# Kernel optimization log

Measured on AMD Instinct MI355X. Metric: run time of the kernel, lower is better.

Reference implementation:

```python
import jax, jax.numpy as jnp
import numpy as np

B, C, CE, H, W = 4, 128, 64, 64, 64
V = H * W
# parent(i) < i//2 guarantees depth <= ceil(log2(V)) = 12; 14 is a safe static bound
MAX_LEVELS = 14


def _gather_v(x, idx):
    # x: [B, C, V], idx: [B, V] -> gather along vertex dim (broadcast over C)
    return jnp.take_along_axis(x, idx[:, None, :], axis=2)


def _tree_filter(feature_in, embed_in, sorted_index, sorted_parent, node_level):
    Bv, Cv, Hv, Wv = feature_in.shape
    Vv = Hv * Wv
    f = feature_in.reshape(Bv, Cv, Vv)
    e = embed_in.reshape(Bv, embed_in.shape[1], Vv)
    # build_edge_weight: gather to BFS order, gather parent, squared-L2 distance, exp(-d)
    f_s = _gather_v(f, sorted_index)          # [B,C,V] features in topological order
    e_s = _gather_v(e, sorted_index)
    e_p = _gather_v(e_s, sorted_parent)
    d2 = jnp.sum((e_s - e_p) ** 2, axis=1)    # [B,V]
    w = jnp.exp(-d2)                          # edge weight node->parent (root: exp(0)=1, unused)
    wB = w[:, None, :]
    # ---- up sweep (leaves -> root), level-parallel over BFS levels ----
    # A_i = f_i + sum_{c in child(i)} w_c * A_c ; Z_i = 1 + sum w_c * Z_c (self_weight = 1)
    aggr_up = f_s
    nrm_up = jnp.ones((Bv, Vv), feature_in.dtype)
    for d in range(MAX_LEVELS - 1, 0, -1):
        mw = jnp.where(node_level == d, w, jnp.zeros((), feature_in.dtype))
        aggr_up = jax.vmap(lambda a, p, m: a.at[:, p].add(m))(
            aggr_up, sorted_parent, mw[:, None, :] * aggr_up)
        nrm_up = jax.vmap(lambda a, p, m: a.at[p].add(m))(
            nrm_up, sorted_parent, mw * nrm_up)
    # ---- down sweep (root -> leaves) ----
    # Ahat_i = A_i + w_i * (Ahat_parent - w_i * A_i); root keeps A_root
    aggr = aggr_up
    nrm = nrm_up
    for d in range(1, MAX_LEVELS):
        sel = node_level == d
        pa = _gather_v(aggr, sorted_parent)
        aggr = jnp.where(sel[:, None, :], aggr_up + wB * (pa - wB * aggr_up), aggr)
        pn = jnp.take_along_axis(nrm, sorted_parent, axis=1)
        nrm = jnp.where(sel, nrm_up + w * (pn - w * nrm_up), nrm)
    out_s = aggr / nrm[:, None, :]
    # scatter back from BFS order to original vertex order
    out = jax.vmap(lambda o, i: jnp.zeros_like(o).at[:, i].set(o))(out_s, sorted_index)
    return out.reshape(Bv, Cv, Hv, Wv)


def setup_inputs() -> dict:
    key = jax.random.key(0)
    k1, k2 = jax.random.split(key)
    feature_in = jax.random.normal(k1, (B, C, H, W), dtype=jnp.float32)
    embed_in = 0.1 * jax.random.normal(k2, (B, CE, H, W), dtype=jnp.float32)
    rng = np.random.default_rng(0)
    sorted_index = np.stack([rng.permutation(V) for _ in range(B)]).astype(np.int32)
    sorted_parent = np.zeros((B, V), dtype=np.int32)
    node_level = np.zeros((B, V), dtype=np.int32)
    for b in range(B):
        for i in range(1, V):
            p = int(rng.integers(0, max(1, i // 2)))  # parent earlier in order, depth <= log2(V)
            sorted_parent[b, i] = p
            node_level[b, i] = node_level[b, p] + 1
    return {
        "feature_in": feature_in,
        "embed_in": embed_in,
        "sorted_index": jnp.asarray(sorted_index),
        "sorted_parent": jnp.asarray(sorted_parent),
        "node_level": jnp.asarray(node_level),
    }


def reference(feature_in, embed_in, sorted_index, sorted_parent, node_level):
    return _tree_filter(feature_in, embed_in, sorted_index, sorted_parent, node_level)
```

## Files before the change

kernel.cpp:

```cpp
#include <hip/hip_runtime.h>

#define BB 4
#define CC 128
#define CE 64
#define VV 4096
#define NLEV 14


__device__ __forceinline__ void lds_fadd(float* p, float v) {
    unsafeAtomicAdd(p, v);
}

__global__ __launch_bounds__(256) void prep_kernel(
    const float* __restrict__ embed,
    const int* __restrict__ sorted_index,
    const int* __restrict__ sorted_parent,
    const int* __restrict__ node_level,
    float* __restrict__ wsort,
    int*   __restrict__ giInv,
    int2*  __restrict__ cpl,
    int*   __restrict__ offs)
{
    int tid = threadIdx.x;
    if (blockIdx.x < BB) {
        int b = blockIdx.x;
        __shared__ int  pos_s[VV];
        __shared__ int4 cntv[NLEV * 64];
        __shared__ int  tot[NLEV];
        __shared__ int  offSh[NLEV + 1];
        int* cnt = (int*)cntv;
        const int* lev = node_level    + b * VV;
        const int* si  = sorted_index  + b * VV;
        const int* par = sorted_parent + b * VV;
        int lane = tid & 63;
        int w    = tid >> 6;

        int dreg[16], sreg[16];
        #pragma unroll
        for (int t = 0; t < 4; ++t) {
            int4 dv = ((const int4*)lev)[tid * 4 + t];
            int4 sv = ((const int4*)si)[tid * 4 + t];
            #pragma unroll
            for (int j = 0; j < 4; ++j) {
                int d = (&dv.x)[j]; d = d < NLEV - 1 ? d : NLEV - 1;
                dreg[t * 4 + j] = d;
                sreg[t * 4 + j] = (&sv.x)[j];
            }
        }

        int rank[16];
        #pragma unroll
        for (int m = 0; m < 16; ++m) {
            int r = 0;
            #pragma unroll
            for (int m2 = 0; m2 < m; ++m2) r += (dreg[m2] == dreg[m]) ? 1 : 0;
            rank[m] = r;
        }

        #pragma unroll
        for (int d = 0; d < NLEV; ++d) {
            int c = 0;
            #pragma unroll
            for (int m = 0; m < 16; ++m) c += (dreg[m] == d) ? 1 : 0;
            cnt[d * 256 + tid] = c;
        }
        __syncthreads();

        for (int d = w; d < NLEV; d += 4) {
            int base = d * 64 + lane;
            int4 cv = cntv[base];
            int ls = cv.x + cv.y + cv.z + cv.w;
            int x = ls;
            #pragma unroll
            for (int off = 1; off < 64; off <<= 1) {
                int y = __shfl_up(x, off, 64);
                if (lane >= off) x += y;
            }
            int excl = x - ls;
            int4 ov;
            ov.x = excl;
            ov.y = excl + cv.x;
            ov.z = excl + cv.x + cv.y;
            ov.w = excl + cv.x + cv.y + cv.z;
            cntv[base] = ov;
            if (lane == 63) tot[d] = x;
        }
        __syncthreads();
        if (tid == 0) {
            int acc = 0;
            for (int d = 0; d < NLEV; ++d) { offSh[d] = acc; acc += tot[d]; }
            offSh[NLEV] = acc;
        }
        __syncthreads();
        if (tid <= NLEV) offs[b * 16 + tid] = offSh[tid];

        int kreg[16];
        #pragma unroll
        for (int m = 0; m < 16; ++m) {
            int d = dreg[m];
            int k = offSh[d] + cnt[d * 256 + tid] + rank[m];
            kreg[m] = k;
            pos_s[16 * tid + m] = k;
            giInv[b * VV + sreg[m]] = k;
        }
        __syncthreads();

        #pragma unroll
        for (int t = 0; t < 4; ++t) {
            int4 pv = ((const int4*)par)[tid * 4 + t];
            #pragma unroll
            for (int j = 0; j < 4; ++j) {
                int m = t * 4 + j;
                int p = (&pv.x)[j];
                cpl[b * VV + kreg[m]] = make_int2(pos_s[p], 16 * tid + m);
            }
        }
    } else {
        __shared__ float part[4][64];
        int bb   = blockIdx.x - BB;
        int b    = bb >> 6;
        int n0   = (bb & 63) << 6;
        int lane = tid & 63;
        int w    = tid >> 6;
        int i    = n0 + lane;
        int vi = sorted_index[b * VV + i];
        int p  = sorted_parent[b * VV + i];
        int vp = sorted_index[b * VV + p];
        const float* eb = embed + (size_t)b * CE * VV;
        float acc = 0.f;
        #pragma unroll
        for (int r = 0; r < 16; ++r) {
            int ce = w * 16 + r;
            float d = eb[ce * VV + vi] - eb[ce * VV + vp];
            acc = fmaf(d, d, acc);
        }
        part[w][lane] = acc;
        __syncthreads();
        if (w == 0) {
            float d2 = part[0][lane] + part[1][lane] + part[2][lane] + part[3][lane];
            wsort[b * VV + i] = __expf(-d2);
        }
    }
}

__global__ __launch_bounds__(512) void tree2_kernel(
    const float* __restrict__ feat,
    const float* __restrict__ wsort,
    const int*  __restrict__ giInv,
    const int2* __restrict__ cpl,
    const int*  __restrict__ offs,
    float* __restrict__ out)
{
    __shared__ float val0[VV];
    __shared__ float val1[VV];
    __shared__ float nrm[VV];
    __shared__ int   cw[VV];
    __shared__ int   offS[16];
    int b   = blockIdx.x >> 6;
    int c0  = (blockIdx.x & 63) << 1;
    int tid = threadIdx.x;

    const int2*  cplB = cpl   + b * VV;
    const int*   ivB  = giInv + b * VV;
    const float* wsB  = wsort + b * VV;
    const float* f0   = feat + ((size_t)(b * CC + c0)) * VV;
    const float* f1   = f0 + VV;

    if (tid < 16) offS[tid] = offs[b * 16 + tid];

    #pragma unroll
    for (int t = 0; t < 8; ++t) {
        int k = tid + t * 512;
        int2 x = cplB[k];
        int wb = __float_as_int(wsB[x.y]);
        cw[k] = (wb & 0xFFFFF000) | x.x;
    }

    int4 kkR[2];
    #pragma unroll
    for (int t = 0; t < 2; ++t) {
        int idx = tid + t * 512;
        int4   kk = ((const int4*)ivB)[idx];
        float4 a  = ((const float4*)f0)[idx];
        float4 bq = ((const float4*)f1)[idx];
        kkR[t] = kk;
        val0[kk.x] = a.x;  val0[kk.y] = a.y;  val0[kk.z] = a.z;  val0[kk.w] = a.w;
        val1[kk.x] = bq.x; val1[kk.y] = bq.y; val1[kk.z] = bq.z; val1[kk.w] = bq.w;
        nrm[kk.x] = 1.f;   nrm[kk.y] = 1.f;   nrm[kk.z] = 1.f;   nrm[kk.w] = 1.f;
    }
    __syncthreads();

    for (int d = NLEV - 1; d >= 1; --d) {
        int s = offS[d], e = offS[d + 1];
        if (s == e) continue;
        for (int k = s + tid; k < e; k += 512) {
            int x = cw[k];
            float w = __int_as_float(x & 0xFFFFF000);
            int  cp = x & 0xFFF;
            lds_fadd(&val0[cp], w * val0[k]);
            lds_fadd(&val1[cp], w * val1[k]);
            lds_fadd(&nrm[cp],  w * nrm[k]);
        }
        __syncthreads();
    }

    for (int d = 1; d <= NLEV - 1; ++d) {
        int s = offS[d], e = offS[d + 1];
        if (s == e) continue;
        for (int k = s + tid; k < e; k += 512) {
            int x = cw[k];
            float w = __int_as_float(x & 0xFFFFF000);
            int  cp = x & 0xFFF;
            float u0 = val0[k], u1 = val1[k], un = nrm[k];
            val0[k] = fmaf(w, fmaf(-w, u0, val0[cp]), u0);
            val1[k] = fmaf(w, fmaf(-w, u1, val1[cp]), u1);
            nrm[k]  = fmaf(w, fmaf(-w, un, nrm[cp]),  un);
        }
        __syncthreads();
    }

    float* o0 = out + ((size_t)(b * CC + c0)) * VV;
    float* o1 = o0 + VV;
    #pragma unroll
    for (int t = 0; t < 2; ++t) {
        int idx = tid + t * 512;
        int4 kk = kkR[t];
        float i0 = __fdividef(1.f, nrm[kk.x]);
        float i1 = __fdividef(1.f, nrm[kk.y]);
        float i2 = __fdividef(1.f, nrm[kk.z]);
        float i3 = __fdividef(1.f, nrm[kk.w]);
        float4 r0, r1;
        r0.x = val0[kk.x] * i0; r0.y = val0[kk.y] * i1;
        r0.z = val0[kk.z] * i2; r0.w = val0[kk.w] * i3;
        r1.x = val1[kk.x] * i0; r1.y = val1[kk.y] * i1;
        r1.z = val1[kk.z] * i2; r1.w = val1[kk.w] * i3;
        ((float4*)o0)[idx] = r0;
        ((float4*)o1)[idx] = r1;
    }
}

extern "C" void kernel_launch(void* const* d_in, const int* in_sizes, int n_in,
                              void* d_out, int out_size, void* d_ws, size_t ws_size,
                              hipStream_t stream) {
    const float* feat          = (const float*)d_in[0];
    const float* embed         = (const float*)d_in[1];
    const int*   sorted_index  = (const int*)d_in[2];
    const int*   sorted_parent = (const int*)d_in[3];
    const int*   node_level    = (const int*)d_in[4];
    float* out = (float*)d_out;

    char* ws = (char*)d_ws;
    const size_t A = (size_t)BB * VV * 4;
    float* wsort = (float*)(ws);
    int*   giInv = (int*)  (ws + A);
    int2*  cpl   = (int2*) (ws + 2 * A);
    int*   offs  = (int*)  (ws + 4 * A);

    prep_kernel<<<BB + BB * 64, 256, 0, stream>>>(
        embed, sorted_index, sorted_parent, node_level, wsort, giInv, cpl, offs);

    tree2_kernel<<<BB * CC / 2, 512, 0, stream>>>(
        feat, wsort, giInv, cpl, offs, out);
}
```

Baseline: 103.3 us.

## Share tree normalizer across channel blocks and fuse edge-weight compute into tree kernel

```diff
diff --git a/kernel.cpp b/kernel.cpp
--- a/kernel.cpp
+++ b/kernel.cpp
@@ -10,20 +10,31 @@
 __device__ __forceinline__ void lds_fadd(float* p, float v) {
     unsafeAtomicAdd(p, v);
 }
+__device__ __forceinline__ float agent_loadf(const float* p) {
+    return __hip_atomic_load(p, __ATOMIC_RELAXED, __HIP_MEMORY_SCOPE_AGENT);
+}
+__device__ __forceinline__ void agent_storef(float* p, float v) {
+    __hip_atomic_store(p, v, __ATOMIC_RELAXED, __HIP_MEMORY_SCOPE_AGENT);
+}
+__device__ __forceinline__ int agent_loadi(const int* p) {
+    return __hip_atomic_load(p, __ATOMIC_RELAXED, __HIP_MEMORY_SCOPE_AGENT);
+}
 
 __global__ __launch_bounds__(256) void prep_kernel(
     const float* __restrict__ embed,
     const int* __restrict__ sorted_index,
     const int* __restrict__ sorted_parent,
     const int* __restrict__ node_level,
-    float* __restrict__ wsort,
     int*   __restrict__ giInv,
     int2*  __restrict__ cpl,
-    int*   __restrict__ offs)
+    int*   __restrict__ offs,
+    int*   __restrict__ sync,
+    float* __restrict__ embedT)
 {
     int tid = threadIdx.x;
     if (blockIdx.x < BB) {
         int b = blockIdx.x;
+        if (tid == 0) { sync[b] = 0; sync[4 + b] = 0; }
         __shared__ int  pos_s[VV];
         __shared__ int4 cntv[NLEV * 64];
         __shared__ int  tot[NLEV];
@@ -47,7 +58,6 @@
                 sreg[t * 4 + j] = (&sv.x)[j];
             }
         }
-
         int rank[16];
         #pragma unroll
         for (int m = 0; m < 16; ++m) {
@@ -56,7 +66,6 @@
             for (int m2 = 0; m2 < m; ++m2) r += (dreg[m2] == dreg[m]) ? 1 : 0;
             rank[m] = r;
         }
-
         #pragma unroll
         for (int d = 0; d < NLEV; ++d) {
             int c = 0;
@@ -65,7 +74,6 @@
             cnt[d * 256 + tid] = c;
         }
         __syncthreads();
-
         for (int d = w; d < NLEV; d += 4) {
             int base = d * 64 + lane;
             int4 cv = cntv[base];
@@ -93,7 +101,6 @@
         }
         __syncthreads();
         if (tid <= NLEV) offs[b * 16 + tid] = offSh[tid];
-
         int kreg[16];
         #pragma unroll
         for (int m = 0; m < 16; ++m) {
@@ -104,7 +111,6 @@
             giInv[b * VV + sreg[m]] = k;
         }
         __syncthreads();
-
         #pragma unroll
         for (int t = 0; t < 4; ++t) {
             int4 pv = ((const int4*)par)[tid * 4 + t];
@@ -116,77 +122,195 @@
             }
         }
     } else {
-        __shared__ float part[4][64];
-        int bb   = blockIdx.x - BB;
-        int b    = bb >> 6;
-        int n0   = (bb & 63) << 6;
-        int lane = tid & 63;
-        int w    = tid >> 6;
-        int i    = n0 + lane;
-        int vi = sorted_index[b * VV + i];
-        int p  = sorted_parent[b * VV + i];
-        int vp = sorted_index[b * VV + p];
-        const float* eb = embed + (size_t)b * CE * VV;
-        float acc = 0.f;
-        #pragma unroll
-        for (int r = 0; r < 16; ++r) {
-            int ce = w * 16 + r;
-            float d = eb[ce * VV + vi] - eb[ce * VV + vp];
-            acc = fmaf(d, d, acc);
-        }
-        part[w][lane] = acc;
-        __syncthreads();
-        if (w == 0) {
-            float d2 = part[0][lane] + part[1][lane] + part[2][lane] + part[3][lane];
-            wsort[b * VV + i] = __expf(-d2);
-        }
-    }
-}
-
-__global__ __launch_bounds__(512) void tree2_kernel(
+        __shared__ float tile[64][65];
+        int tb = blockIdx.x - BB;
+        int b  = tb >> 6;
+        int v0 = (tb & 63) << 6;
+        const float* eb  = embed  + (size_t)b * CE * VV;
+        float*       ebT = embedT + (size_t)b * VV * CE;
+        int cv = tid & 63;
+        int rh = tid >> 6;
+        #pragma unroll
+        for (int it = 0; it < 16; ++it) {
+            int ce = it * 4 + rh;
+            tile[cv][ce] = eb[(size_t)ce * VV + v0 + cv];
+        }
+        __syncthreads();
+        #pragma unroll
+        for (int it = 0; it < 16; ++it) {
+            int dv = it * 4 + rh;
+            ebT[(size_t)(v0 + dv) * CE + cv] = tile[dv][cv];
+        }
+    }
+}
+
+__global__ __launch_bounds__(512, 4) void tree2_kernel(
     const float* __restrict__ feat,
-    const float* __restrict__ wsort,
+    const float* __restrict__ embedT,
+    const int*  __restrict__ sorted_index,
+    const int*  __restrict__ sorted_parent,
+    float* __restrict__ wsort,
     const int*  __restrict__ giInv,
     const int2* __restrict__ cpl,
     const int*  __restrict__ offs,
+    int*   __restrict__ sync,
+    float* __restrict__ nrmInv,
     float* __restrict__ out)
 {
     __shared__ float val0[VV];
     __shared__ float val1[VV];
-    __shared__ float nrm[VV];
     __shared__ int   cw[VV];
     __shared__ int   offS[16];
-    int b   = blockIdx.x >> 6;
-    int c0  = (blockIdx.x & 63) << 1;
     int tid = threadIdx.x;
+
+    if (blockIdx.x < BB) {
+        int b = blockIdx.x;
+        const int2* cplB = cpl + b * VV;
+        if (tid < 16) offS[tid] = offs[b * 16 + tid];
+        #pragma unroll
+        for (int t = 0; t < 8; ++t) {
+            int k = tid + t * 512;
+            int2 x = cplB[k];
+            cw[k] = x.x | (x.y << 12);
+        }
+        if (tid == 0) {
+            while (agent_loadi(&sync[b]) < 64) __builtin_amdgcn_s_sleep(1);
+        }
+        __syncthreads();
+        __threadfence();
+        #pragma unroll
+        for (int t = 0; t < 8; ++t) {
+            int k = tid + t * 512;
+            val0[k] = agent_loadf(&wsort[b * VV + k]);
+        }
+        __syncthreads();
+        #pragma unroll
+        for (int t = 0; t < 8; ++t) {
+            int k = tid + t * 512;
+            int pk = cw[k];
+            int iy = (pk >> 12) & 0xFFF;
+            int wb = __float_as_int(val0[iy]);
+            cw[k] = (wb & 0xFFFFF000) | (pk & 0xFFF);
+        }
+        __syncthreads();
+        #pragma unroll
+        for (int t = 0; t < 8; ++t) val0[tid + t * 512] = 1.f;
+        __syncthreads();
+        for (int d = NLEV - 1; d >= 1; --d) {
+            int s = offS[d], e = offS[d + 1];
+            if (s == e) continue;
+            for (int k = s + tid; k < e; k += 512) {
+                int x = cw[k];
+                float w = __int_as_float(x & 0xFFFFF000);
+                int  cp = x & 0xFFF;
+                lds_fadd(&val0[cp], w * val0[k]);
+            }
+            __syncthreads();
+        }
+        for (int d = 1; d <= NLEV - 1; ++d) {
+            int s = offS[d], e = offS[d + 1];
+            if (s == e) continue;
+            for (int k = s + tid; k < e; k += 512) {
+                int x = cw[k];
+                float w = __int_as_float(x & 0xFFFFF000);
+                int  cp = x & 0xFFF;
+                float un = val0[k];
+                val0[k] = fmaf(w, fmaf(-w, un, val0[cp]), un);
+            }
+            __syncthreads();
+        }
+        #pragma unroll
+        for (int t = 0; t < 8; ++t) {
+            int k = tid + t * 512;
+            agent_storef(&nrmInv[b * VV + k], __fdividef(1.f, val0[k]));
+        }
+        __threadfence();
+        __syncthreads();
+        if (tid == 0) __hip_atomic_store(&sync[4 + b], 1, __ATOMIC_RELAXED, __HIP_MEMORY_SCOPE_AGENT);
+        return;
+    }
+
+    int tb = blockIdx.x - BB;
+    int b  = tb >> 6;
+    int j  = tb & 63;
+    int c0 = j << 1;
 
     const int2*  cplB = cpl   + b * VV;
     const int*   ivB  = giInv + b * VV;
-    const float* wsB  = wsort + b * VV;
     const float* f0   = feat + ((size_t)(b * CC + c0)) * VV;
     const float* f1   = f0 + VV;
 
+    {
+        int n   = tid >> 3;
+        int sub = tid & 7;
+        int i   = (j << 6) + n;
+        int vi = sorted_index[b * VV + i];
+        int p  = sorted_parent[b * VV + i];
+        int vp = sorted_index[b * VV + p];
+        const float4* ra = (const float4*)(embedT + ((size_t)b * VV + vi) * CE);
+        const float4* rb = (const float4*)(embedT + ((size_t)b * VV + vp) * CE);
+        float4 a0 = ra[sub * 2], a1 = ra[sub * 2 + 1];
+        float4 b0 = rb[sub * 2], b1 = rb[sub * 2 + 1];
+        float d2 = 0.f, t0;
+        t0 = a0.x - b0.x; d2 = fmaf(t0, t0, d2);
+        t0 = a0.y - b0.y; d2 = fmaf(t0, t0, d2);
+        t0 = a0.z - b0.z; d2 = fmaf(t0, t0, d2);
+        t0 = a0.w - b0.w; d2 = fmaf(t0, t0, d2);
+        t0 = a1.x - b1.x; d2 = fmaf(t0, t0, d2);
+        t0 = a1.y - b1.y; d2 = fmaf(t0, t0, d2);
+        t0 = a1.z - b1.z; d2 = fmaf(t0, t0, d2);
+        t0 = a1.w - b1.w; d2 = fmaf(t0, t0, d2);
+        d2 += __shfl_xor(d2, 1, 64);
+        d2 += __shfl_xor(d2, 2, 64);
+        d2 += __shfl_xor(d2, 4, 64);
+        if (sub == 0) agent_storef(&wsort[b * VV + i], __expf(-d2));
+    }
+    __threadfence();
+    __syncthreads();
+    if (tid == 0) __hip_atomic_fetch_add(&sync[b], 1, __ATOMIC_RELAXED, __HIP_MEMORY_SCOPE_AGENT);
+
     if (tid < 16) offS[tid] = offs[b * 16 + tid];
-
+    int4   kkR[2];
+    float4 fA[2], fB[2];
+    #pragma unroll
+    for (int t = 0; t < 2; ++t) {
+        int idx = tid + t * 512;
+        kkR[t] = ((const int4*)ivB)[idx];
+        fA[t]  = ((const float4*)f0)[idx];
+        fB[t]  = ((const float4*)f1)[idx];
+    }
     #pragma unroll
     for (int t = 0; t < 8; ++t) {
         int k = tid + t * 512;
         int2 x = cplB[k];
-        int wb = __float_as_int(wsB[x.y]);
-        cw[k] = (wb & 0xFFFFF000) | x.x;
-    }
-
-    int4 kkR[2];
+        cw[k] = x.x | (x.y << 12);
+    }
+
+    if (tid == 0) {
+        while (agent_loadi(&sync[b]) < 64) __builtin_amdgcn_s_sleep(1);
+    }
+    __syncthreads();
+    __threadfence();
+    #pragma unroll
+    for (int t = 0; t < 8; ++t) {
+        int k = tid + t * 512;
+        val0[k] = agent_loadf(&wsort[b * VV + k]);
+    }
+    __syncthreads();
+    #pragma unroll
+    for (int t = 0; t < 8; ++t) {
+        int k = tid + t * 512;
+        int pk = cw[k];
+        int iy = (pk >> 12) & 0xFFF;
+        int wb = __float_as_int(val0[iy]);
+        cw[k] = (wb & 0xFFFFF000) | (pk & 0xFFF);
+    }
+    __syncthreads();
     #pragma unroll
     for (int t = 0; t < 2; ++t) {
-        int idx = tid + t * 512;
-        int4   kk = ((const int4*)ivB)[idx];
-        float4 a  = ((const float4*)f0)[idx];
-        float4 bq = ((const float4*)f1)[idx];
-        kkR[t] = kk;
-        val0[kk.x] = a.x;  val0[kk.y] = a.y;  val0[kk.z] = a.z;  val0[kk.w] = a.w;
-        val1[kk.x] = bq.x; val1[kk.y] = bq.y; val1[kk.z] = bq.z; val1[kk.w] = bq.w;
-        nrm[kk.x] = 1.f;   nrm[kk.y] = 1.f;   nrm[kk.z] = 1.f;   nrm[kk.w] = 1.f;
+        int4 kk = kkR[t];
+        val0[kk.x] = fA[t].x; val0[kk.y] = fA[t].y; val0[kk.z] = fA[t].z; val0[kk.w] = fA[t].w;
+        val1[kk.x] = fB[t].x; val1[kk.y] = fB[t].y; val1[kk.z] = fB[t].z; val1[kk.w] = fB[t].w;
     }
     __syncthreads();
 
@@ -199,11 +323,9 @@
             int  cp = x & 0xFFF;
             lds_fadd(&val0[cp], w * val0[k]);
             lds_fadd(&val1[cp], w * val1[k]);
-            lds_fadd(&nrm[cp],  w * nrm[k]);
-        }
-        __syncthreads();
-    }
-
+        }
+        __syncthreads();
+    }
     for (int d = 1; d <= NLEV - 1; ++d) {
         int s = offS[d], e = offS[d + 1];
         if (s == e) continue;
@@ -211,13 +333,25 @@
             int x = cw[k];
             float w = __int_as_float(x & 0xFFFFF000);
             int  cp = x & 0xFFF;
-            float u0 = val0[k], u1 = val1[k], un = nrm[k];
+            float u0 = val0[k], u1 = val1[k];
             val0[k] = fmaf(w, fmaf(-w, u0, val0[cp]), u0);
             val1[k] = fmaf(w, fmaf(-w, u1, val1[cp]), u1);
-            nrm[k]  = fmaf(w, fmaf(-w, un, nrm[cp]),  un);
-        }
-        __syncthreads();
-    }
+        }
+        __syncthreads();
+    }
+
+    if (tid == 0) {
+        while (agent_loadi(&sync[4 + b]) == 0) __builtin_amdgcn_s_sleep(1);
+    }
+    __syncthreads();
+    __threadfence();
+    float* nv = (float*)cw;
+    #pragma unroll
+    for (int t = 0; t < 8; ++t) {
+        int k = tid + t * 512;
+        nv[k] = agent_loadf(&nrmInv[b * VV + k]);
+    }
+    __syncthreads();
 
     float* o0 = out + ((size_t)(b * CC + c0)) * VV;
     float* o1 = o0 + VV;
@@ -225,10 +359,7 @@
     for (int t = 0; t < 2; ++t) {
         int idx = tid + t * 512;
         int4 kk = kkR[t];
-        float i0 = __fdividef(1.f, nrm[kk.x]);
-        float i1 = __fdividef(1.f, nrm[kk.y]);
-        float i2 = __fdividef(1.f, nrm[kk.z]);
-        float i3 = __fdividef(1.f, nrm[kk.w]);
+        float i0 = nv[kk.x], i1 = nv[kk.y], i2 = nv[kk.z], i3 = nv[kk.w];
         float4 r0, r1;
         r0.x = val0[kk.x] * i0; r0.y = val0[kk.y] * i1;
         r0.z = val0[kk.z] * i2; r0.w = val0[kk.w] * i3;
@@ -251,14 +382,17 @@
 
     char* ws = (char*)d_ws;
     const size_t A = (size_t)BB * VV * 4;
-    float* wsort = (float*)(ws);
-    int*   giInv = (int*)  (ws + A);
-    int2*  cpl   = (int2*) (ws + 2 * A);
-    int*   offs  = (int*)  (ws + 4 * A);
-
-    prep_kernel<<<BB + BB * 64, 256, 0, stream>>>(
-        embed, sorted_index, sorted_parent, node_level, wsort, giInv, cpl, offs);
-
-    tree2_kernel<<<BB * CC / 2, 512, 0, stream>>>(
-        feat, wsort, giInv, cpl, offs, out);
-}
+    float* wsort  = (float*)(ws);
+    int*   giInv  = (int*)  (ws + A);
+    int2*  cpl    = (int2*) (ws + 2 * A);
+    int*   offs   = (int*)  (ws + 4 * A);
+    int*   sync   = (int*)  (ws + 4 * A + 4096);
+    float* nrmInv = (float*)(ws + 5 * A);
+    float* embedT = (float*)(ws + 6 * A);
+
+    prep_kernel<<<BB + 256, 256, 0, stream>>>(
+        embed, sorted_index, sorted_parent, node_level, giInv, cpl, offs, sync, embedT);
+
+    tree2_kernel<<<BB + 256, 512, 0, stream>>>(
+        feat, embedT, sorted_index, sorted_parent, wsort, giInv, cpl, offs, sync, nrmInv, out);
+}
```

After: 205.3 us. 98.7% more time.

## Process one channel per block and prefetch next tree level's edges

Applied to the files above, without the earlier changes.

```diff
diff --git a/kernel.cpp b/kernel.cpp
--- a/kernel.cpp
+++ b/kernel.cpp
@@ -47,7 +47,6 @@
                 sreg[t * 4 + j] = (&sv.x)[j];
             }
         }
-
         int rank[16];
         #pragma unroll
         for (int m = 0; m < 16; ++m) {
@@ -56,7 +55,6 @@
             for (int m2 = 0; m2 < m; ++m2) r += (dreg[m2] == dreg[m]) ? 1 : 0;
             rank[m] = r;
         }
-
         #pragma unroll
         for (int d = 0; d < NLEV; ++d) {
             int c = 0;
@@ -65,7 +63,6 @@
             cnt[d * 256 + tid] = c;
         }
         __syncthreads();
-
         for (int d = w; d < NLEV; d += 4) {
             int base = d * 64 + lane;
             int4 cv = cntv[base];
@@ -93,7 +90,6 @@
         }
         __syncthreads();
         if (tid <= NLEV) offs[b * 16 + tid] = offSh[tid];
-
         int kreg[16];
         #pragma unroll
         for (int m = 0; m < 16; ++m) {
@@ -104,7 +100,6 @@
             giInv[b * VV + sreg[m]] = k;
         }
         __syncthreads();
-
         #pragma unroll
         for (int t = 0; t < 4; ++t) {
             int4 pv = ((const int4*)par)[tid * 4 + t];
@@ -143,7 +138,7 @@
     }
 }
 
-__global__ __launch_bounds__(512) void tree2_kernel(
+__global__ __launch_bounds__(512, 4) void tree1_kernel(
     const float* __restrict__ feat,
     const float* __restrict__ wsort,
     const int*  __restrict__ giInv,
@@ -151,20 +146,18 @@
     const int*  __restrict__ offs,
     float* __restrict__ out)
 {
-    __shared__ float val0[VV];
-    __shared__ float val1[VV];
+    __shared__ float val[VV];
     __shared__ float nrm[VV];
     __shared__ int   cw[VV];
     __shared__ int   offS[16];
-    int b   = blockIdx.x >> 6;
-    int c0  = (blockIdx.x & 63) << 1;
+    int b   = blockIdx.x >> 7;
+    int c   = blockIdx.x & 127;
     int tid = threadIdx.x;
 
     const int2*  cplB = cpl   + b * VV;
     const int*   ivB  = giInv + b * VV;
     const float* wsB  = wsort + b * VV;
-    const float* f0   = feat + ((size_t)(b * CC + c0)) * VV;
-    const float* f1   = f0 + VV;
+    const float* f0   = feat + ((size_t)(b * CC + c)) * VV;
 
     if (tid < 16) offS[tid] = offs[b * 16 + tid];
 
@@ -174,6 +167,7 @@
         int2 x = cplB[k];
         int wb = __float_as_int(wsB[x.y]);
         cw[k] = (wb & 0xFFFFF000) | x.x;
+        nrm[k] = 1.f;
     }
 
     int4 kkR[2];
@@ -182,60 +176,84 @@
         int idx = tid + t * 512;
         int4   kk = ((const int4*)ivB)[idx];
         float4 a  = ((const float4*)f0)[idx];
-        float4 bq = ((const float4*)f1)[idx];
         kkR[t] = kk;
-        val0[kk.x] = a.x;  val0[kk.y] = a.y;  val0[kk.z] = a.z;  val0[kk.w] = a.w;
-        val1[kk.x] = bq.x; val1[kk.y] = bq.y; val1[kk.z] = bq.z; val1[kk.w] = bq.w;
-        nrm[kk.x] = 1.f;   nrm[kk.y] = 1.f;   nrm[kk.z] = 1.f;   nrm[kk.w] = 1.f;
+        val[kk.x] = a.x; val[kk.y] = a.y; val[kk.z] = a.z; val[kk.w] = a.w;
     }
     __syncthreads();
 
-    for (int d = NLEV - 1; d >= 1; --d) {
-        int s = offS[d], e = offS[d + 1];
-        if (s == e) continue;
-        for (int k = s + tid; k < e; k += 512) {
-            int x = cw[k];
-            float w = __int_as_float(x & 0xFFFFF000);
-            int  cp = x & 0xFFF;
-            lds_fadd(&val0[cp], w * val0[k]);
-            lds_fadd(&val1[cp], w * val1[k]);
-            lds_fadd(&nrm[cp],  w * nrm[k]);
-        }
-        __syncthreads();
-    }
-
-    for (int d = 1; d <= NLEV - 1; ++d) {
-        int s = offS[d], e = offS[d + 1];
-        if (s == e) continue;
-        for (int k = s + tid; k < e; k += 512) {
-            int x = cw[k];
-            float w = __int_as_float(x & 0xFFFFF000);
-            int  cp = x & 0xFFF;
-            float u0 = val0[k], u1 = val1[k], un = nrm[k];
-            val0[k] = fmaf(w, fmaf(-w, u0, val0[cp]), u0);
-            val1[k] = fmaf(w, fmaf(-w, u1, val1[cp]), u1);
-            nrm[k]  = fmaf(w, fmaf(-w, un, nrm[cp]),  un);
-        }
-        __syncthreads();
-    }
-
-    float* o0 = out + ((size_t)(b * CC + c0)) * VV;
-    float* o1 = o0 + VV;
+    {
+        int sN = offS[NLEV - 1], eN = offS[NLEV];
+        int kN = sN + tid;
+        int xN = (kN < eN) ? cw[kN] : 0;
+        for (int d = NLEV - 1; d >= 1; --d) {
+            int s = sN, e = eN, x0 = xN;
+            sN = offS[d - 1]; eN = offS[d];
+            kN = sN + tid;
+            xN = (kN < eN) ? cw[kN] : 0;
+            int k = s + tid;
+            if (k < e) {
+                float w = __int_as_float(x0 & 0xFFFFF000);
+                int  cp = x0 & 0xFFF;
+                lds_fadd(&val[cp], w * val[k]);
+                lds_fadd(&nrm[cp], w * nrm[k]);
+                for (k += 512; k < e; k += 512) {
+                    int x = cw[k];
+                    w  = __int_as_float(x & 0xFFFFF000);
+                    cp = x & 0xFFF;
+                    lds_fadd(&val[cp], w * val[k]);
+                    lds_fadd(&nrm[cp], w * nrm[k]);
+                }
+            }
+            __syncthreads();
+        }
+    }
+
+    {
+        int sN = offS[1], eN = offS[2];
+        int kN = sN + tid;
+        bool vN = kN < eN;
+        int   xN = vN ? cw[kN]  : 0;
+        float uN = vN ? val[kN] : 0.f;
+        float nN = vN ? nrm[kN] : 0.f;
+        for (int d = 1; d <= NLEV - 1; ++d) {
+            int s = sN, e = eN, x0 = xN;
+            float u0 = uN, n0 = nN;
+            sN = offS[d + 1]; eN = offS[d + 2 <= NLEV ? d + 2 : NLEV];
+            kN = sN + tid;
+            bool v2 = (d + 1 <= NLEV - 1) && (kN < eN);
+            xN = v2 ? cw[kN]  : 0;
+            uN = v2 ? val[kN] : 0.f;
+            nN = v2 ? nrm[kN] : 0.f;
+            int k = s + tid;
+            if (k < e) {
+                float w = __int_as_float(x0 & 0xFFFFF000);
+                int  cp = x0 & 0xFFF;
+                val[k] = fmaf(w, fmaf(-w, u0, val[cp]), u0);
+                nrm[k] = fmaf(w, fmaf(-w, n0, nrm[cp]), n0);
+                for (k += 512; k < e; k += 512) {
+                    int x = cw[k];
+                    w  = __int_as_float(x & 0xFFFFF000);
+                    cp = x & 0xFFF;
+                    float u = val[k], n = nrm[k];
+                    val[k] = fmaf(w, fmaf(-w, u, val[cp]), u);
+                    nrm[k] = fmaf(w, fmaf(-w, n, nrm[cp]), n);
+                }
+            }
+            __syncthreads();
+        }
+    }
+
+    float* o0 = out + ((size_t)(b * CC + c)) * VV;
     #pragma unroll
     for (int t = 0; t < 2; ++t) {
         int idx = tid + t * 512;
         int4 kk = kkR[t];
-        float i0 = __fdividef(1.f, nrm[kk.x]);
-        float i1 = __fdividef(1.f, nrm[kk.y]);
-        float i2 = __fdividef(1.f, nrm[kk.z]);
-        float i3 = __fdividef(1.f, nrm[kk.w]);
-        float4 r0, r1;
-        r0.x = val0[kk.x] * i0; r0.y = val0[kk.y] * i1;
-        r0.z = val0[kk.z] * i2; r0.w = val0[kk.w] * i3;
-        r1.x = val1[kk.x] * i0; r1.y = val1[kk.y] * i1;
-        r1.z = val1[kk.z] * i2; r1.w = val1[kk.w] * i3;
+        float4 r0;
+        r0.x = __fdividef(val[kk.x], nrm[kk.x]);
+        r0.y = __fdividef(val[kk.y], nrm[kk.y]);
+        r0.z = __fdividef(val[kk.z], nrm[kk.z]);
+        r0.w = __fdividef(val[kk.w], nrm[kk.w]);
         ((float4*)o0)[idx] = r0;
-        ((float4*)o1)[idx] = r1;
     }
 }
 
@@ -259,6 +277,6 @@
     prep_kernel<<<BB + BB * 64, 256, 0, stream>>>(
         embed, sorted_index, sorted_parent, node_level, wsort, giInv, cpl, offs);
 
-    tree2_kernel<<<BB * CC / 2, 512, 0, stream>>>(
+    tree1_kernel<<<BB * CC, 512, 0, stream>>>(
         feat, wsort, giInv, cpl, offs, out);
 }
```

Result: slower. 111.1 us (+7.5%).
